# Kernel tuning notes

Measured on AMD Instinct MI355X. Metric: run time of the kernel, lower is better.

Reference implementation:

```python
import jax, jax.numpy as jnp
import numpy as np

B, H, W, C = 4, 256, 256, 96
NH, WIN = 3, 8
HD = C // NH
HID = 4 * C
SCALE = HD ** -0.5
N = WIN * WIN


def _rel_pos_index(win):
    # matches torch.meshgrid([h, w]) default 'ij' indexing
    coords = np.stack(np.meshgrid(np.arange(win), np.arange(win), indexing='ij'))
    cf = coords.reshape(2, -1)
    rel = (cf[:, :, None] - cf[:, None, :]).transpose(1, 2, 0).astype(np.int64)
    rel[..., 0] += win - 1
    rel[..., 1] += win - 1
    rel[..., 0] *= 2 * win - 1
    return rel.sum(-1)

REL_IDX = jnp.asarray(_rel_pos_index(WIN))


def _ln(x, g, b, eps=1e-5):
    m = x.mean(-1, keepdims=True)
    v = ((x - m) ** 2).mean(-1, keepdims=True)
    return (x - m) * jax.lax.rsqrt(v + eps) * g + b


def setup_inputs() -> dict:
    key = jax.random.key(0)
    ks = jax.random.split(key, 10)
    s = 0.02
    return {
        'x': jax.random.normal(ks[0], (B, H * W, C), jnp.float32),
        'g1': jnp.ones((C,), jnp.float32), 'b1': jnp.zeros((C,), jnp.float32),
        'wq': jax.random.normal(ks[1], (C, C), jnp.float32) * s, 'bq': jnp.zeros((C,), jnp.float32),
        'wkv': jax.random.normal(ks[2], (C, 2 * C), jnp.float32) * s, 'bkv': jnp.zeros((2 * C,), jnp.float32),
        'rpb': jax.random.normal(ks[3], ((2 * WIN - 1) ** 2, NH), jnp.float32) * s,
        'wp': jax.random.normal(ks[4], (C, C), jnp.float32) * s, 'bp': jnp.zeros((C,), jnp.float32),
        'g2': jnp.ones((C,), jnp.float32), 'b2': jnp.zeros((C,), jnp.float32),
        'w1': jax.random.normal(ks[5], (C, HID), jnp.float32) * s, 'bl1': jnp.zeros((HID,), jnp.float32),
        'wdw': jax.random.normal(ks[6], (HID, 1, 3, 3), jnp.float32) * s, 'bdw': jnp.zeros((HID,), jnp.float32),
        'w2': jax.random.normal(ks[7], (HID, C), jnp.float32) * s, 'bl2': jnp.zeros((C,), jnp.float32),
    }


def reference(x, g1, b1, wq, bq, wkv, bkv, rpb, wp, bp, g2, b2, w1, bl1, wdw, bdw, w2, bl2):
    shortcut = x
    xn = _ln(x, g1, b1)
    q = xn @ wq + bq                      # (B, L, C)
    kv = xn @ wkv + bkv                   # (B, L, 2C)

    def windows(t, c):
        t = t.reshape(B, H // WIN, WIN, W // WIN, WIN, c)
        return t.transpose(0, 1, 3, 2, 4, 5).reshape(-1, N, c)

    qw = windows(q, C).reshape(-1, N, NH, HD).transpose(0, 2, 1, 3)     # (nB, NH, N, HD)
    kvw = windows(kv, 2 * C).reshape(-1, N, 2, NH, HD).transpose(2, 0, 3, 1, 4)
    kw, vw = kvw[0], kvw[1]

    attn = jnp.einsum('bhnd,bhmd->bhnm', qw * SCALE, kw)                # (nB, NH, N, N)
    bias = rpb[REL_IDX]                                                  # (N, N, NH)
    attn = attn + bias.transpose(2, 0, 1)[None]
    # shift_size=0 -> shift mask is identically zero; adding it is a no-op
    attn = jax.nn.softmax(attn, axis=-1)
    y = jnp.einsum('bhnm,bhmd->bhnd', attn, vw)
    y = y.transpose(0, 2, 1, 3).reshape(-1, N, C)
    y = y @ wp + bp

    # window_reverse
    y = y.reshape(B, H // WIN, W // WIN, WIN, WIN, C)
    y = y.transpose(0, 1, 3, 2, 4, 5).reshape(B, H * W, C)
    x = shortcut + y

    # LeFF: linear1 + GELU -> depthwise 3x3 conv + GELU -> linear2
    xn2 = _ln(x, g2, b2)
    h = jax.nn.gelu(xn2 @ w1 + bl1, approximate=False)                  # (B, L, HID)
    h = h.reshape(B, H, W, HID).transpose(0, 3, 1, 2)                    # NCHW
    h = jax.lax.conv_general_dilated(
        h, wdw, window_strides=(1, 1), padding=((1, 1), (1, 1)),
        dimension_numbers=('NCHW', 'OIHW', 'NCHW'), feature_group_count=HID)
    h = jax.nn.gelu(h + bdw[None, :, None, None], approximate=False)
    h = h.transpose(0, 2, 3, 1).reshape(B, H * W, HID)
    h = h @ w2 + bl2
    return x + h
```

## Files before the change

### kernel.cpp

```cpp
#include <hip/hip_runtime.h>
#include <math.h>


typedef __attribute__((ext_vector_type(8))) short bf16x8;
typedef __attribute__((ext_vector_type(4))) float f32x4;
typedef __attribute__((ext_vector_type(2))) float f32x2;

#define MFMA(a, b, c) __builtin_amdgcn_mfma_f32_16x16x32_bf16((a), (b), (c), 0, 0, 0)

#define WQ_T 0
#define WKV_T 18
#define WP_T 54
#define W1_T 72
#define W2_T 144
#define NTILES_TOT 216

__device__ __forceinline__ unsigned short f2bf(float f) {
  union { float f; unsigned u; } v; v.f = f;
  unsigned r = v.u + 0x7FFFu + ((v.u >> 16) & 1u);
  return (unsigned short)(r >> 16);
}
__device__ __forceinline__ float asf(unsigned u) {
  union { unsigned u; float f; } v; v.u = u; return v.f;
}
__device__ __forceinline__ unsigned cvtpk_bf16(float lo, float hi) {
  unsigned r;
  asm("v_cvt_pk_bf16_f32 %0, %1, %2" : "=v"(r) : "v"(lo), "v"(hi));
  return r;
}
__device__ __forceinline__ float gelu(float x) {
  float a = __expf(-1.702f * x);
  return x * __builtin_amdgcn_rcpf(1.f + a);
}
__device__ __forceinline__ bf16x8 ldw(const unsigned short* wswz, int tile, int lane) {
  return *(const bf16x8*)(wswz + ((size_t)(tile * 64 + lane)) * 8);
}
__device__ __forceinline__ int xcd_swz(int bid) {
  return (bid & 7) * 512 + (bid >> 3);
}

__global__ void kwconv(const float* __restrict__ wq, const float* __restrict__ wkv,
                       const float* __restrict__ wp, const float* __restrict__ w1,
                       const float* __restrict__ w2, const float* __restrict__ wdw,
                       unsigned short* __restrict__ wswz, float* __restrict__ wdwT) {
  int tid = blockIdx.x * 256 + threadIdx.x;
  if (tid >= NTILES_TOT * 64) {
    int i = tid - NTILES_TOT * 64;
    if (i < 3456) {
      int ch = i % 384, tap = i / 384;
      wdwT[tap * 384 + ch] = wdw[ch * 9 + tap];
    }
    return;
  }
  int e = tid; const float* src; int N, NT;
  if (e < 1152)      { src = wq;  N = 96;  NT = 6; }
  else if (e < 3456) { src = wkv; N = 192; NT = 12; e -= 1152; }
  else if (e < 4608) { src = wp;  N = 96;  NT = 6;  e -= 3456; }
  else if (e < 9216) { src = w1;  N = 384; NT = 24; e -= 4608; }
  else               { src = w2;  N = 96;  NT = 6;  e -= 9216; }
  int lane = e & 63, t = e >> 6;
  int nt = t % NT, kt = t / NT;
  int k0 = kt * 32 + (lane >> 4) * 8;
  int n = nt * 16 + (lane & 15);
  unsigned short* dst = wswz + (size_t)tid * 8;
#pragma unroll
  for (int i = 0; i < 8; ++i) dst[i] = f2bf(src[(size_t)(k0 + i) * N + n]);
}

__global__ __launch_bounds__(256) void kattn(
    const float* __restrict__ x, const float* __restrict__ g1, const float* __restrict__ b1,
    const float* __restrict__ bq, const float* __restrict__ bkv,
    const float* __restrict__ rpb, const float* __restrict__ bp,
    const unsigned short* __restrict__ wswz, float* __restrict__ x2) {
  __shared__ __align__(16) unsigned short sm0[4 * 3 * 64 * 8];
  __shared__ __align__(16) unsigned short sm1[24 * 64 * 8];
  __shared__ __align__(16) unsigned short sm2[3 * 2 * 2 * 64 * 8];

  const int tid = threadIdx.x;
  const int lane = tid & 63, w = tid >> 6;
  const int lrow = lane >> 4, lcol = lane & 15;
  const int wi = xcd_swz(blockIdx.x);
  const int b = wi >> 10, wy = (wi >> 5) & 31, wx = wi & 31;

  long rowoff[4];
#pragma unroll
  for (int r = 0; r < 4; ++r) {
    int m = w * 16 + lrow * 4 + r;
    int gy = wy * 8 + (m >> 3), gx = wx * 8 + (m & 7);
    rowoff[r] = ((long)b * 65536 + gy * 256 + gx) * 96;
  }

  float xv[4][6], xn[4][6], gv[6], bv[6];
#pragma unroll
  for (int nt = 0; nt < 6; ++nt) {
    int c = nt * 16 + lcol;
    gv[nt] = g1[c]; bv[nt] = b1[c];
#pragma unroll
    for (int r = 0; r < 4; ++r) xv[r][nt] = x[rowoff[r] + c];
  }
#pragma unroll
  for (int r = 0; r < 4; ++r) {
    float s = 0.f, sq = 0.f;
#pragma unroll
    for (int nt = 0; nt < 6; ++nt) { float v = xv[r][nt]; s += v; sq += v * v; }
#pragma unroll
    for (int off = 1; off <= 8; off <<= 1) { s += __shfl_xor(s, off, 64); sq += __shfl_xor(sq, off, 64); }
    float mean = s * (1.f / 96.f);
    float var = sq * (1.f / 96.f) - mean * mean;
    float rs = rsqrtf(var + 1e-5f);
#pragma unroll
    for (int nt = 0; nt < 6; ++nt) xn[r][nt] = (xv[r][nt] - mean) * rs * gv[nt] + bv[nt];
  }
#pragma unroll
  for (int r = 0; r < 4; ++r) {
    int mm = lrow * 4 + r;
#pragma unroll
    for (int nt = 0; nt < 6; ++nt) {
      int c = nt * 16 + lcol;
      int kt = c >> 5;
      int lanew = mm + (((c & 31) >> 3) << 4);
      sm0[((w * 3 + kt) * 64 + lanew) * 8 + (c & 7)] = f2bf(xn[r][nt]);
    }
  }

  bf16x8 af[3];
#pragma unroll
  for (int kt = 0; kt < 3; ++kt) af[kt] = *(const bf16x8*)(sm0 + ((w * 3 + kt) * 64 + lane) * 8);
  for (int nt = 0; nt < 18; ++nt) {
    f32x4 acc = {0.f, 0.f, 0.f, 0.f};
    if (nt < 12) {
#pragma unroll
      for (int kt = 0; kt < 3; ++kt) {
        int tile = (nt < 6) ? (WQ_T + kt * 6 + nt) : (WKV_T + kt * 12 + (nt - 6));
        acc = MFMA(ldw(wswz, tile, lane), af[kt], acc);
      }
      if (nt < 6) {
        int cq = nt * 16 + lrow * 4;
        f32x4 b4 = *(const f32x4*)(bq + cq);
        int head = cq >> 5, d0 = cq & 31;
        unsigned p0 = cvtpk_bf16((acc.x + b4.x) * 0.17677669529663687f,
                                 (acc.y + b4.y) * 0.17677669529663687f);
        unsigned p1 = cvtpk_bf16((acc.z + b4.z) * 0.17677669529663687f,
                                 (acc.w + b4.w) * 0.17677669529663687f);
        uint2 uv = {p0, p1};
        *(uint2*)(sm1 + (((head * 4 + w) * 64) + lcol + ((d0 >> 3) << 4)) * 8 + (d0 & 7)) = uv;
      } else {
        int ck = (nt - 6) * 16 + lrow * 4;
        f32x4 b4 = *(const f32x4*)(bkv + ck);
        int head = ck >> 5, d0 = ck & 31;
        unsigned p0 = cvtpk_bf16(acc.x + b4.x, acc.y + b4.y);
        unsigned p1 = cvtpk_bf16(acc.z + b4.z, acc.w + b4.w);
        uint2 uv = {p0, p1};
        *(uint2*)(sm1 + ((12 + head * 4 + w) * 64 + lcol + ((d0 >> 3) << 4)) * 8 + (d0 & 7)) = uv;
      }
    } else {
#pragma unroll
      for (int kt = 0; kt < 3; ++kt)
        acc = MFMA(af[kt], ldw(wswz, WKV_T + kt * 12 + (nt - 6), lane), acc);
      int vc = (nt - 12) * 16 + lcol;
      float bvv = bkv[96 + vc];
      int head = vc >> 5, nt2 = (vc >> 4) & 1;
      int m0 = w * 16 + lrow * 4;
      unsigned p0 = cvtpk_bf16(acc.x + bvv, acc.y + bvv);
      unsigned p1 = cvtpk_bf16(acc.z + bvv, acc.w + bvv);
      uint2 uv = {p0, p1};
      *(uint2*)(sm2 + ((((head * 2 + (m0 >> 5)) * 2 + nt2) * 64) + lcol +
                       (((m0 & 31) >> 3) << 4)) * 8 + (m0 & 7)) = uv;
    }
  }
  __syncthreads();

  f32x4 sc[3][4];
#pragma unroll
  for (int uu = 0; uu < 3; ++uu) {
    int u = w * 3 + uu, head = u >> 2, mtq = u & 3;
    bf16x8 aq = *(const bf16x8*)(sm1 + ((head * 4 + mtq) * 64 + lane) * 8);
#pragma unroll
    for (int nt = 0; nt < 4; ++nt) {
      bf16x8 bk = *(const bf16x8*)(sm1 + ((12 + head * 4 + nt) * 64 + lane) * 8);
      f32x4 z = {0.f, 0.f, 0.f, 0.f};
      sc[uu][nt] = MFMA(bk, aq, z);
    }
  }
  __syncthreads();

#pragma unroll
  for (int uu = 0; uu < 3; ++uu) {
    int u = w * 3 + uu, head = u >> 2, mtq = u & 3;
    const int qtok = mtq * 16 + lcol;
    const int qdy = (qtok >> 3), qdx = (qtok & 7);
#pragma unroll
    for (int nt = 0; nt < 4; ++nt) {
#pragma unroll
      for (int r = 0; r < 4; ++r) {
        int ktok = nt * 16 + lrow * 4 + r;
        int dy = qdy - (ktok >> 3) + 7;
        int dx = qdx - (ktok & 7) + 7;
        sc[uu][nt][r] += rpb[(dy * 15 + dx) * 3 + head];
      }
    }
    float mx = sc[uu][0][0];
#pragma unroll
    for (int nt = 0; nt < 4; ++nt)
#pragma unroll
      for (int r = 0; r < 4; ++r) mx = fmaxf(mx, sc[uu][nt][r]);
    mx = fmaxf(mx, __shfl_xor(mx, 16, 64));
    mx = fmaxf(mx, __shfl_xor(mx, 32, 64));
    float sum = 0.f;
#pragma unroll
    for (int nt = 0; nt < 4; ++nt)
#pragma unroll
      for (int r = 0; r < 4; ++r) { sc[uu][nt][r] = __expf(sc[uu][nt][r] - mx); sum += sc[uu][nt][r]; }
    sum += __shfl_xor(sum, 16, 64);
    sum += __shfl_xor(sum, 32, 64);
    float inv = 1.f / sum;
    const int ebase = (lrow & 1) * 4;
    const int hi = (lrow >> 1);
#pragma unroll
    for (int nt = 0; nt < 4; ++nt) {
      unsigned p0 = cvtpk_bf16(sc[uu][nt][0] * inv, sc[uu][nt][1] * inv);
      unsigned p1 = cvtpk_bf16(sc[uu][nt][2] * inv, sc[uu][nt][3] * inv);
      uint2 uv = {p0, p1};
      *(uint2*)(sm1 + ((((head * 4 + mtq) * 2 + (nt >> 1)) * 64) + lcol +
                       ((((nt & 1) * 2 + hi)) << 4)) * 8 + ebase) = uv;
    }
  }

#pragma unroll
  for (int uu = 0; uu < 3; ++uu) {
    int u = w * 3 + uu, head = u >> 2, mtq = u & 3;
#pragma unroll
    for (int nt2 = 0; nt2 < 2; ++nt2) {
      f32x4 acc = {0.f, 0.f, 0.f, 0.f};
#pragma unroll
      for (int ktile = 0; ktile < 2; ++ktile) {
        bf16x8 ap = *(const bf16x8*)(sm1 + (((head * 4 + mtq) * 2 + ktile) * 64 + lane) * 8);
        bf16x8 bv8 = *(const bf16x8*)(sm2 + (((head * 2 + ktile) * 2 + nt2) * 64 + lane) * 8);
        acc = MFMA(bv8, ap, acc);
      }
      unsigned p0 = cvtpk_bf16(acc.x, acc.y);
      unsigned p1 = cvtpk_bf16(acc.z, acc.w);
      uint2 uv = {p0, p1};
      *(uint2*)(sm0 + ((mtq * 3 + head) * 64 + lcol +
                       ((nt2 * 2 + (lrow >> 1)) << 4)) * 8 + (lrow & 1) * 4) = uv;
    }
  }
  __syncthreads();

  bf16x8 ay[3];
#pragma unroll
  for (int kt = 0; kt < 3; ++kt) ay[kt] = *(const bf16x8*)(sm0 + ((w * 3 + kt) * 64 + lane) * 8);
#pragma unroll
  for (int nt = 0; nt < 6; ++nt) {
    f32x4 acc = {0.f, 0.f, 0.f, 0.f};
#pragma unroll
    for (int kt = 0; kt < 3; ++kt) acc = MFMA(ay[kt], ldw(wswz, WP_T + kt * 6 + nt, lane), acc);
    int c = nt * 16 + lcol;
    float bpc = bp[c];
#pragma unroll
    for (int r = 0; r < 4; ++r) x2[rowoff[r] + c] = acc[r] + bpc + xv[r][nt];
  }
}

__device__ __forceinline__ bf16x8 dwconv_gelu_g(
    const unsigned short* h00,
    const float* __restrict__ wdwT, const float* __restrict__ bdw, int ch) {
  f32x2 a2[4];
#pragma unroll
  for (int j = 0; j < 4; ++j) a2[j] = (f32x2){0.f, 0.f};
#pragma unroll
  for (int dy = 0; dy < 3; ++dy) {
    uint4 dv[3];
#pragma unroll
    for (int dx = 0; dx < 3; ++dx)
      dv[dx] = *(const uint4*)(h00 + (dy * 10 + dx) * 200);
#pragma unroll
    for (int dx = 0; dx < 3; ++dx) {
      int t = dy * 3 + dx;
      f32x4 wlo = *(const f32x4*)(wdwT + t * 384 + ch);
      f32x4 whi = *(const f32x4*)(wdwT + t * 384 + ch + 4);
      const unsigned* du = (const unsigned*)&dv[dx];
      f32x2 d0 = { asf(du[0] << 16), asf(du[0] & 0xffff0000u) };
      f32x2 d1 = { asf(du[1] << 16), asf(du[1] & 0xffff0000u) };
      f32x2 d2 = { asf(du[2] << 16), asf(du[2] & 0xffff0000u) };
      f32x2 d3 = { asf(du[3] << 16), asf(du[3] & 0xffff0000u) };
      f32x2 w0 = {wlo.x, wlo.y}, w1 = {wlo.z, wlo.w};
      f32x2 w2v = {whi.x, whi.y}, w3 = {whi.z, whi.w};
      a2[0] += d0 * w0; a2[1] += d1 * w1; a2[2] += d2 * w2v; a2[3] += d3 * w3;
    }
  }
  f32x4 blo = *(const f32x4*)(bdw + ch);
  f32x4 bhi = *(const f32x4*)(bdw + ch + 4);
  union { unsigned u[4]; bf16x8 v; } pk;
  pk.u[0] = cvtpk_bf16(gelu(a2[0].x + blo.x), gelu(a2[0].y + blo.y));
  pk.u[1] = cvtpk_bf16(gelu(a2[1].x + blo.z), gelu(a2[1].y + blo.w));
  pk.u[2] = cvtpk_bf16(gelu(a2[2].x + bhi.x), gelu(a2[2].y + bhi.y));
  pk.u[3] = cvtpk_bf16(gelu(a2[3].x + bhi.z), gelu(a2[3].y + bhi.w));
  return pk.v;
}

__global__ __launch_bounds__(256) void kleff(
    const float* __restrict__ x2, const float* __restrict__ g2,
    const float* __restrict__ b2, const float* __restrict__ bl1,
    const float* __restrict__ wdwT, const float* __restrict__ bdw,
    const float* __restrict__ bl2, const unsigned short* __restrict__ wswz,
    float* __restrict__ out) {
  __shared__ __align__(16) unsigned short smem[100 * 200];

  const int tid = threadIdx.x, lane = tid & 63, w = tid >> 6;
  const int lrow = lane >> 4, lcol = lane & 15;
  const int bid = xcd_swz(blockIdx.x);
  const int b = bid >> 10, ty0 = ((bid >> 5) & 31) * 8, tx0 = (bid & 31) * 8;

  const int mt1 = (w < 3) ? 4 + w : 3;

  {
    float2 gv2[3], bv2[3];
#pragma unroll
    for (int n3 = 0; n3 < 3; ++n3) {
      gv2[n3] = *(const float2*)(g2 + n3 * 32 + lcol * 2);
      bv2[n3] = *(const float2*)(b2 + n3 * 32 + lcol * 2);
    }
#pragma unroll
    for (int mi = 0; mi < 2; ++mi) {
      const int mt = mi ? mt1 : w;
      float2 xv[4][3];
#pragma unroll
      for (int r = 0; r < 4; ++r) {
        int t = mt * 16 + lrow * 4 + r;
        int hy = (t * 205) >> 11, hx = t - hy * 10;
        int gy = ty0 - 1 + hy, gx = tx0 - 1 + hx;
        int cgy = min(max(gy, 0), 255), cgx = min(max(gx, 0), 255);
        long roff = ((long)b * 65536 + cgy * 256 + cgx) * 96;
#pragma unroll
        for (int n3 = 0; n3 < 3; ++n3)
          xv[r][n3] = *(const float2*)(x2 + roff + n3 * 32 + lcol * 2);
      }
#pragma unroll
      for (int r = 0; r < 4; ++r) {
        float s = 0.f, sq = 0.f;
#pragma unroll
        for (int n3 = 0; n3 < 3; ++n3) {
          float2 v = xv[r][n3];
          s += v.x + v.y; sq += v.x * v.x + v.y * v.y;
        }
#pragma unroll
        for (int off = 1; off <= 8; off <<= 1) { s += __shfl_xor(s, off, 64); sq += __shfl_xor(sq, off, 64); }
        float mean = s * (1.f / 96.f);
        float var = sq * (1.f / 96.f) - mean * mean;
        float rs = rsqrtf(var + 1e-5f);
        int mm = lrow * 4 + r;
#pragma unroll
        for (int n3 = 0; n3 < 3; ++n3) {
          float vx = (xv[r][n3].x - mean) * rs * gv2[n3].x + bv2[n3].x;
          float vy = (xv[r][n3].y - mean) * rs * gv2[n3].y + bv2[n3].y;
          unsigned pk = cvtpk_bf16(vx, vy);
          *(unsigned*)(smem + ((mt * 3 + n3) * 64 + mm + ((lcol >> 2) << 4)) * 8 +
                       ((lcol * 2) & 7)) = pk;
        }
      }
    }
  }

  bf16x8 af0[3], af1[3];
#pragma unroll
  for (int kt = 0; kt < 3; ++kt) {
    af0[kt] = *(const bf16x8*)(smem + ((w * 3 + kt) * 64 + lane) * 8);
    af1[kt] = *(const bf16x8*)(smem + ((mt1 * 3 + kt) * 64 + lane) * 8);
  }
  __syncthreads();

  const int tA = w * 16 + lcol;
  const int tB = mt1 * 16 + lcol;
  bool okA, okB;
  {
    int hy = (tA * 205) >> 11, hx = tA - hy * 10;
    int gy = ty0 - 1 + hy, gx = tx0 - 1 + hx;
    okA = ((unsigned)gy < 256u) && ((unsigned)gx < 256u);
    hy = (tB * 205) >> 11; hx = tB - hy * 10;
    gy = ty0 - 1 + hy; gx = tx0 - 1 + hx;
    okB = ((unsigned)gy < 256u) && ((unsigned)gx < 256u) && (tB < 100);
  }
  const bool stB = (tB < 100);

  f32x4 acc[6];
#pragma unroll
  for (int nt = 0; nt < 6; ++nt) { f32x4 z = {0.f, 0.f, 0.f, 0.f}; acc[nt] = z; }

  const int pint = w * 16 + lcol;
  const int iy = pint >> 3, ix = pint & 7;

#pragma unroll
  for (int H = 0; H < 2; ++H) {
#pragma unroll
    for (int ntl = 0; ntl < 12; ++ntl) {
      int nt = H * 12 + ntl;
      bf16x8 wf0 = ldw(wswz, W1_T + nt, lane);
      bf16x8 wf1 = ldw(wswz, W1_T + 24 + nt, lane);
      bf16x8 wf2 = ldw(wswz, W1_T + 48 + nt, lane);
      int ct0 = ntl * 16 + lrow * 4;
      f32x4 b4 = *(const f32x4*)(bl1 + H * 192 + ct0);
      f32x4 a0 = {0.f, 0.f, 0.f, 0.f}, a1 = {0.f, 0.f, 0.f, 0.f};
      a0 = MFMA(wf0, af0[0], a0); a0 = MFMA(wf1, af0[1], a0); a0 = MFMA(wf2, af0[2], a0);
      a1 = MFMA(wf0, af1[0], a1); a1 = MFMA(wf1, af1[1], a1); a1 = MFMA(wf2, af1[2], a1);
      unsigned p0 = cvtpk_bf16(gelu(a0.x + b4.x), gelu(a0.y + b4.y));
      unsigned p1 = cvtpk_bf16(gelu(a0.z + b4.z), gelu(a0.w + b4.w));
      uint2 uvA = { okA ? p0 : 0u, okA ? p1 : 0u };
      *(uint2*)(smem + tA * 200 + ct0) = uvA;
      unsigned q0 = cvtpk_bf16(gelu(a1.x + b4.x), gelu(a1.y + b4.y));
      unsigned q1 = cvtpk_bf16(gelu(a1.z + b4.z), gelu(a1.w + b4.w));
      if (stB) {
        uint2 uvB = { okB ? q0 : 0u, okB ? q1 : 0u };
        *(uint2*)(smem + tB * 200 + ct0) = uvB;
      }
    }
    __syncthreads();

#pragma unroll
    for (int ktl = 0; ktl < 6; ++ktl) {
      const int ktg = H * 6 + ktl;
      const int choff = ktl * 32 + lrow * 8;
      const unsigned short* h00 = smem + (iy * 10 + ix) * 200 + choff;
      bf16x8 pk = dwconv_gelu_g(h00, wdwT, bdw, H * 192 + choff);
#pragma unroll
      for (int nt = 0; nt < 6; ++nt)
        acc[nt] = MFMA(pk, ldw(wswz, W2_T + ktg * 6 + nt, lane), acc[nt]);
    }
    __syncthreads();
  }

#pragma unroll
  for (int nt = 0; nt < 6; ++nt) {
    int c = nt * 16 + lcol;
    float bb = bl2[c];
#pragma unroll
    for (int r = 0; r < 4; ++r) {
      int mm = w * 16 + lrow * 4 + r;
      int oy = ty0 + (mm >> 3), ox = tx0 + (mm & 7);
      long row = (long)b * 65536 + oy * 256 + ox;
      out[row * 96 + c] = acc[nt][r] + bb + x2[row * 96 + c];
    }
  }
}

extern "C" void kernel_launch(void* const* d_in, const int* in_sizes, int n_in,
                              void* d_out, int out_size, void* d_ws, size_t ws_size,
                              hipStream_t stream) {
  const float* x   = (const float*)d_in[0];
  const float* g1  = (const float*)d_in[1];
  const float* b1  = (const float*)d_in[2];
  const float* wq  = (const float*)d_in[3];
  const float* bq  = (const float*)d_in[4];
  const float* wkv = (const float*)d_in[5];
  const float* bkv = (const float*)d_in[6];
  const float* rpb = (const float*)d_in[7];
  const float* wp  = (const float*)d_in[8];
  const float* bp  = (const float*)d_in[9];
  const float* g2  = (const float*)d_in[10];
  const float* b2  = (const float*)d_in[11];
  const float* w1  = (const float*)d_in[12];
  const float* bl1 = (const float*)d_in[13];
  const float* wdw = (const float*)d_in[14];
  const float* bdw = (const float*)d_in[15];
  const float* w2  = (const float*)d_in[16];
  const float* bl2 = (const float*)d_in[17];

  char* ws = (char*)d_ws;
  unsigned short* wswz = (unsigned short*)ws;
  float* wdwT = (float*)(ws + (size_t)(256 << 10));
  float* x2 = (float*)(ws + (size_t)(4 << 20));
  float* outp = (float*)d_out;

  kwconv<<<68, 256, 0, stream>>>(wq, wkv, wp, w1, w2, wdw, wswz, wdwT);
  kattn<<<4096, 256, 0, stream>>>(x, g1, b1, bq, bkv, rpb, bp, wswz, x2);
  kleff<<<4096, 256, 0, stream>>>(x2, g2, b2, bl1, wdwT, bdw, bl2, wswz, outp);
}
```

Baseline: 458.6 us.

## Split LeFF block across eight waves with K-split reduction through shared memory

```diff
diff --git a/kernel.cpp b/kernel.cpp
--- a/kernel.cpp
+++ b/kernel.cpp
@@ -299,7 +299,7 @@
   return pk.v;
 }
 
-__global__ __launch_bounds__(256) void kleff(
+__global__ __launch_bounds__(512, 8) void kleff(
     const float* __restrict__ x2, const float* __restrict__ g2,
     const float* __restrict__ b2, const float* __restrict__ bl1,
     const float* __restrict__ wdwT, const float* __restrict__ bdw,
@@ -312,112 +312,101 @@
   const int bid = xcd_swz(blockIdx.x);
   const int b = bid >> 10, ty0 = ((bid >> 5) & 31) * 8, tx0 = (bid & 31) * 8;
 
-  const int mt1 = (w < 3) ? 4 + w : 3;
-
-  {
+  if (w < 7) {
     float2 gv2[3], bv2[3];
 #pragma unroll
     for (int n3 = 0; n3 < 3; ++n3) {
       gv2[n3] = *(const float2*)(g2 + n3 * 32 + lcol * 2);
       bv2[n3] = *(const float2*)(b2 + n3 * 32 + lcol * 2);
     }
-#pragma unroll
-    for (int mi = 0; mi < 2; ++mi) {
-      const int mt = mi ? mt1 : w;
-      float2 xv[4][3];
-#pragma unroll
-      for (int r = 0; r < 4; ++r) {
-        int t = mt * 16 + lrow * 4 + r;
-        int hy = (t * 205) >> 11, hx = t - hy * 10;
-        int gy = ty0 - 1 + hy, gx = tx0 - 1 + hx;
-        int cgy = min(max(gy, 0), 255), cgx = min(max(gx, 0), 255);
-        long roff = ((long)b * 65536 + cgy * 256 + cgx) * 96;
-#pragma unroll
-        for (int n3 = 0; n3 < 3; ++n3)
-          xv[r][n3] = *(const float2*)(x2 + roff + n3 * 32 + lcol * 2);
-      }
-#pragma unroll
-      for (int r = 0; r < 4; ++r) {
-        float s = 0.f, sq = 0.f;
-#pragma unroll
-        for (int n3 = 0; n3 < 3; ++n3) {
-          float2 v = xv[r][n3];
-          s += v.x + v.y; sq += v.x * v.x + v.y * v.y;
-        }
-#pragma unroll
-        for (int off = 1; off <= 8; off <<= 1) { s += __shfl_xor(s, off, 64); sq += __shfl_xor(sq, off, 64); }
-        float mean = s * (1.f / 96.f);
-        float var = sq * (1.f / 96.f) - mean * mean;
-        float rs = rsqrtf(var + 1e-5f);
-        int mm = lrow * 4 + r;
-#pragma unroll
-        for (int n3 = 0; n3 < 3; ++n3) {
-          float vx = (xv[r][n3].x - mean) * rs * gv2[n3].x + bv2[n3].x;
-          float vy = (xv[r][n3].y - mean) * rs * gv2[n3].y + bv2[n3].y;
-          unsigned pk = cvtpk_bf16(vx, vy);
-          *(unsigned*)(smem + ((mt * 3 + n3) * 64 + mm + ((lcol >> 2) << 4)) * 8 +
-                       ((lcol * 2) & 7)) = pk;
-        }
-      }
-    }
-  }
-
-  bf16x8 af0[3], af1[3];
-#pragma unroll
-  for (int kt = 0; kt < 3; ++kt) {
-    af0[kt] = *(const bf16x8*)(smem + ((w * 3 + kt) * 64 + lane) * 8);
-    af1[kt] = *(const bf16x8*)(smem + ((mt1 * 3 + kt) * 64 + lane) * 8);
+    float2 xv[4][3];
+#pragma unroll
+    for (int r = 0; r < 4; ++r) {
+      int t = w * 16 + lrow * 4 + r;
+      int hy = (t * 205) >> 11, hx = t - hy * 10;
+      int gy = ty0 - 1 + hy, gx = tx0 - 1 + hx;
+      int cgy = min(max(gy, 0), 255), cgx = min(max(gx, 0), 255);
+      long roff = ((long)b * 65536 + cgy * 256 + cgx) * 96;
+#pragma unroll
+      for (int n3 = 0; n3 < 3; ++n3)
+        xv[r][n3] = *(const float2*)(x2 + roff + n3 * 32 + lcol * 2);
+    }
+#pragma unroll
+    for (int r = 0; r < 4; ++r) {
+      float s = 0.f, sq = 0.f;
+#pragma unroll
+      for (int n3 = 0; n3 < 3; ++n3) {
+        float2 v = xv[r][n3];
+        s += v.x + v.y; sq += v.x * v.x + v.y * v.y;
+      }
+#pragma unroll
+      for (int off = 1; off <= 8; off <<= 1) { s += __shfl_xor(s, off, 64); sq += __shfl_xor(sq, off, 64); }
+      float mean = s * (1.f / 96.f);
+      float var = sq * (1.f / 96.f) - mean * mean;
+      float rs = rsqrtf(var + 1e-5f);
+      int mm = lrow * 4 + r;
+#pragma unroll
+      for (int n3 = 0; n3 < 3; ++n3) {
+        float vx = (xv[r][n3].x - mean) * rs * gv2[n3].x + bv2[n3].x;
+        float vy = (xv[r][n3].y - mean) * rs * gv2[n3].y + bv2[n3].y;
+        unsigned pk = cvtpk_bf16(vx, vy);
+        *(unsigned*)(smem + ((w * 3 + n3) * 64 + mm + ((lcol >> 2) << 4)) * 8 +
+                     ((lcol * 2) & 7)) = pk;
+      }
+    }
+  }
+
+  bf16x8 af0[3];
+  if (w < 7) {
+#pragma unroll
+    for (int kt = 0; kt < 3; ++kt)
+      af0[kt] = *(const bf16x8*)(smem + ((w * 3 + kt) * 64 + lane) * 8);
   }
   __syncthreads();
 
   const int tA = w * 16 + lcol;
-  const int tB = mt1 * 16 + lcol;
-  bool okA, okB;
+  bool okA;
   {
     int hy = (tA * 205) >> 11, hx = tA - hy * 10;
     int gy = ty0 - 1 + hy, gx = tx0 - 1 + hx;
     okA = ((unsigned)gy < 256u) && ((unsigned)gx < 256u);
-    hy = (tB * 205) >> 11; hx = tB - hy * 10;
-    gy = ty0 - 1 + hy; gx = tx0 - 1 + hx;
-    okB = ((unsigned)gy < 256u) && ((unsigned)gx < 256u) && (tB < 100);
-  }
-  const bool stB = (tB < 100);
+  }
+  const bool stA = (w < 7) && (tA < 100);
 
   f32x4 acc[6];
 #pragma unroll
   for (int nt = 0; nt < 6; ++nt) { f32x4 z = {0.f, 0.f, 0.f, 0.f}; acc[nt] = z; }
 
-  const int pint = w * 16 + lcol;
+  const int pint = (w & 3) * 16 + lcol;
   const int iy = pint >> 3, ix = pint & 7;
+  const int kgrp = w >> 2;
 
 #pragma unroll
   for (int H = 0; H < 2; ++H) {
-#pragma unroll
-    for (int ntl = 0; ntl < 12; ++ntl) {
-      int nt = H * 12 + ntl;
-      bf16x8 wf0 = ldw(wswz, W1_T + nt, lane);
-      bf16x8 wf1 = ldw(wswz, W1_T + 24 + nt, lane);
-      bf16x8 wf2 = ldw(wswz, W1_T + 48 + nt, lane);
-      int ct0 = ntl * 16 + lrow * 4;
-      f32x4 b4 = *(const f32x4*)(bl1 + H * 192 + ct0);
-      f32x4 a0 = {0.f, 0.f, 0.f, 0.f}, a1 = {0.f, 0.f, 0.f, 0.f};
-      a0 = MFMA(wf0, af0[0], a0); a0 = MFMA(wf1, af0[1], a0); a0 = MFMA(wf2, af0[2], a0);
-      a1 = MFMA(wf0, af1[0], a1); a1 = MFMA(wf1, af1[1], a1); a1 = MFMA(wf2, af1[2], a1);
-      unsigned p0 = cvtpk_bf16(gelu(a0.x + b4.x), gelu(a0.y + b4.y));
-      unsigned p1 = cvtpk_bf16(gelu(a0.z + b4.z), gelu(a0.w + b4.w));
-      uint2 uvA = { okA ? p0 : 0u, okA ? p1 : 0u };
-      *(uint2*)(smem + tA * 200 + ct0) = uvA;
-      unsigned q0 = cvtpk_bf16(gelu(a1.x + b4.x), gelu(a1.y + b4.y));
-      unsigned q1 = cvtpk_bf16(gelu(a1.z + b4.z), gelu(a1.w + b4.w));
-      if (stB) {
-        uint2 uvB = { okB ? q0 : 0u, okB ? q1 : 0u };
-        *(uint2*)(smem + tB * 200 + ct0) = uvB;
+    if (w < 7) {
+#pragma unroll
+      for (int ntl = 0; ntl < 12; ++ntl) {
+        int nt = H * 12 + ntl;
+        bf16x8 wf0 = ldw(wswz, W1_T + nt, lane);
+        bf16x8 wf1 = ldw(wswz, W1_T + 24 + nt, lane);
+        bf16x8 wf2 = ldw(wswz, W1_T + 48 + nt, lane);
+        int ct0 = ntl * 16 + lrow * 4;
+        f32x4 b4 = *(const f32x4*)(bl1 + H * 192 + ct0);
+        f32x4 a0 = {0.f, 0.f, 0.f, 0.f};
+        a0 = MFMA(wf0, af0[0], a0); a0 = MFMA(wf1, af0[1], a0); a0 = MFMA(wf2, af0[2], a0);
+        unsigned p0 = cvtpk_bf16(gelu(a0.x + b4.x), gelu(a0.y + b4.y));
+        unsigned p1 = cvtpk_bf16(gelu(a0.z + b4.z), gelu(a0.w + b4.w));
+        if (stA) {
+          uint2 uvA = { okA ? p0 : 0u, okA ? p1 : 0u };
+          *(uint2*)(smem + tA * 200 + ct0) = uvA;
+        }
       }
     }
     __syncthreads();
 
 #pragma unroll
-    for (int ktl = 0; ktl < 6; ++ktl) {
+    for (int j = 0; j < 3; ++j) {
+      const int ktl = kgrp * 3 + j;
       const int ktg = H * 6 + ktl;
       const int choff = ktl * 32 + lrow * 8;
       const unsigned short* h00 = smem + (iy * 10 + ix) * 200 + choff;
@@ -429,16 +418,29 @@
     __syncthreads();
   }
 
-#pragma unroll
-  for (int nt = 0; nt < 6; ++nt) {
-    int c = nt * 16 + lcol;
-    float bb = bl2[c];
-#pragma unroll
-    for (int r = 0; r < 4; ++r) {
-      int mm = w * 16 + lrow * 4 + r;
-      int oy = ty0 + (mm >> 3), ox = tx0 + (mm & 7);
-      long row = (long)b * 65536 + oy * 256 + ox;
-      out[row * 96 + c] = acc[nt][r] + bb + x2[row * 96 + c];
+  float* smemf = (float*)smem;
+  if (w >= 4) {
+#pragma unroll
+    for (int nt = 0; nt < 6; ++nt)
+      *(f32x4*)(smemf + ((w & 3) * 64 + lane) * 24 + nt * 4) = acc[nt];
+  }
+  __syncthreads();
+  if (w < 4) {
+#pragma unroll
+    for (int nt = 0; nt < 6; ++nt)
+      acc[nt] += *(const f32x4*)(smemf + (w * 64 + lane) * 24 + nt * 4);
+
+#pragma unroll
+    for (int nt = 0; nt < 6; ++nt) {
+      int c = nt * 16 + lcol;
+      float bb = bl2[c];
+#pragma unroll
+      for (int r = 0; r < 4; ++r) {
+        int mm = w * 16 + lrow * 4 + r;
+        int oy = ty0 + (mm >> 3), ox = tx0 + (mm & 7);
+        long row = (long)b * 65536 + oy * 256 + ox;
+        out[row * 96 + c] = acc[nt][r] + bb + x2[row * 96 + c];
+      }
     }
   }
 }
@@ -473,5 +475,5 @@
 
   kwconv<<<68, 256, 0, stream>>>(wq, wkv, wp, w1, w2, wdw, wswz, wdwT);
   kattn<<<4096, 256, 0, stream>>>(x, g1, b1, bq, bkv, rpb, bp, wswz, x2);
-  kleff<<<4096, 256, 0, stream>>>(x2, g2, b2, bl1, wdwT, bdw, bl2, wswz, outp);
-}
+  kleff<<<4096, 512, 0, stream>>>(x2, g2, b2, bl1, wdwT, bdw, bl2, wswz, outp);
+}
```

Result: slower. 528.4 us (+15.2%).
